# Optimization experiments

Hardware: AMD Instinct MI355X
Metric: run time of the kernel (lower is better)

Reference implementation:

```python
import jax, jax.numpy as jnp
import numpy as np

B, IN_DIM, HID = 32768, 512, 1024
# fixed triangle graph buffer from the module
SRC = jnp.array([0, 1, 2, 1, 2, 0], dtype=jnp.int32)
TGT = jnp.array([1, 2, 0, 0, 1, 2], dtype=jnp.int32)


def setup_inputs() -> dict:
    key = jax.random.key(0)
    ks = jax.random.split(key, 16)
    s_in = 1.0 / np.sqrt(IN_DIM)
    s_h = 1.0 / np.sqrt(HID)
    return {
        "x": jax.random.normal(ks[0], (B, IN_DIM), jnp.float32),
        # encoder: Linear(IN,HID) -> ReLU -> Linear(HID,HID) -> ReLU
        "enc_w1": jax.random.uniform(ks[1], (IN_DIM, HID), jnp.float32, -s_in, s_in),
        "enc_b1": jax.random.uniform(ks[2], (HID,), jnp.float32, -s_in, s_in),
        "enc_w2": jax.random.uniform(ks[3], (HID, HID), jnp.float32, -s_h, s_h),
        "enc_b2": jax.random.uniform(ks[4], (HID,), jnp.float32, -s_h, s_h),
        "init_nodes": jax.random.normal(ks[5], (3, HID), jnp.float32),
        # GIN layer 1 MLP: Linear -> ReLU -> Linear
        "gin1_w1": jax.random.uniform(ks[6], (HID, HID), jnp.float32, -s_h, s_h),
        "gin1_b1": jax.random.uniform(ks[7], (HID,), jnp.float32, -s_h, s_h),
        "gin1_w2": jax.random.uniform(ks[8], (HID, HID), jnp.float32, -s_h, s_h),
        "gin1_b2": jax.random.uniform(ks[9], (HID,), jnp.float32, -s_h, s_h),
        # GIN layer 2 MLP
        "gin2_w1": jax.random.uniform(ks[10], (HID, HID), jnp.float32, -s_h, s_h),
        "gin2_b1": jax.random.uniform(ks[11], (HID,), jnp.float32, -s_h, s_h),
        "gin2_w2": jax.random.uniform(ks[12], (HID, HID), jnp.float32, -s_h, s_h),
        "gin2_b2": jax.random.uniform(ks[13], (HID,), jnp.float32, -s_h, s_h),
        # decoder: Linear(HID, 1)
        "dec_w": jax.random.uniform(ks[14], (HID, 1), jnp.float32, -s_h, s_h),
        "dec_b": jax.random.uniform(ks[15], (1,), jnp.float32, -s_h, s_h),
    }


def _gin_conv(h, w1, b1, w2, b2):
    # h: [B, 3, H]; sum-aggregate neighbor features along fixed edge list, eps=0
    agg = jnp.zeros_like(h).at[:, TGT, :].add(h[:, SRC, :])
    m = h + agg  # (1+eps)*x + aggregate, eps=0
    m = jax.nn.relu(jnp.einsum('bnh,hk->bnk', m, w1) + b1)
    return jnp.einsum('bnh,hk->bnk', m, w2) + b2


def reference(x, enc_w1, enc_b1, enc_w2, enc_b2, init_nodes,
              gin1_w1, gin1_b1, gin1_w2, gin1_b2,
              gin2_w1, gin2_b1, gin2_w2, gin2_b2,
              dec_w, dec_b):
    # encoder (vectorized over batch)
    e = jax.nn.relu(x @ enc_w1 + enc_b1)
    e = jax.nn.relu(e @ enc_w2 + enc_b2)  # [B, H]
    # per-sample node init, batched: [B, 3, H]
    h = init_nodes[None, :, :] + e[:, None, :]
    h = jax.nn.relu(_gin_conv(h, gin1_w1, gin1_b1, gin1_w2, gin1_b2))
    h = jax.nn.relu(_gin_conv(h, gin2_w1, gin2_b1, gin2_w2, gin2_b2))
    out = (jnp.einsum('bnh,ho->bno', h, dec_w) + dec_b)[..., 0]  # [B, 3]
    return out
```

## Files before the change

### kernel.cpp

```cpp
#include <hip/hip_runtime.h>
#include <stdint.h>

#define AS1 __attribute__((address_space(1)))
#define AS3 __attribute__((address_space(3)))

typedef unsigned short ushort_t;
typedef __attribute__((ext_vector_type(8))) short bf16x8;
typedef __attribute__((ext_vector_type(4))) float f32x4;

__device__ __forceinline__ ushort_t f2bf(float f) {
  union { float f; uint32_t u; } c; c.f = f;
  uint32_t u = c.u;
  return (ushort_t)((u + 0x7fffu + ((u >> 16) & 1u)) >> 16);
}


__global__ __launch_bounds__(256) void k_cvt4(const float* __restrict__ in,
                                              ushort_t* __restrict__ out, int n4) {
  int i = blockIdx.x * blockDim.x + threadIdx.x;
  int stride = gridDim.x * blockDim.x;
  for (; i < n4; i += stride) {
    float4 v = ((const float4*)in)[i];
    ushort4 o;
    o.x = f2bf(v.x); o.y = f2bf(v.y); o.z = f2bf(v.z); o.w = f2bf(v.w);
    ((ushort4*)out)[i] = o;
  }
}

__global__ __launch_bounds__(256) void k_suminit(const float* __restrict__ init,
                                                 float* __restrict__ s) {
  int i = blockIdx.x * 256 + threadIdx.x;
  if (i < 1024) s[i] = init[i] + init[i + 1024] + init[i + 2048];
}

__global__ __launch_bounds__(256) void k_transpose(const float* __restrict__ W,
                                                   ushort_t* __restrict__ Wt,
                                                   int K, int N) {
  __shared__ float tile[32][33];
  int tx = threadIdx.x & 31, ty = threadIdx.x >> 5;
  int n0 = blockIdx.x * 32, k0 = blockIdx.y * 32;
  #pragma unroll
  for (int i = ty; i < 32; i += 8)
    tile[i][tx] = W[(size_t)(k0 + i) * N + (n0 + tx)];
  __syncthreads();
  #pragma unroll
  for (int i = ty; i < 32; i += 8)
    Wt[(size_t)(n0 + i) * K + (k0 + tx)] = f2bf(tile[tx][i]);
}


template <int KT, int EPI>
__global__ __launch_bounds__(256, 2)
void gemm_bt(const ushort_t* __restrict__ A, const ushort_t* __restrict__ Bt,
             const float* __restrict__ bias, const float* __restrict__ extra,
             ushort_t* __restrict__ C, float* __restrict__ part) {
  __shared__ char smem[32768];
  char* smA = smem;
  char* smB = smem + 16384;

  const int nwg = gridDim.x;
  const int cpx = nwg >> 3;
  int bid = blockIdx.x;
  int wg = (bid & 7) * cpx + (bid >> 3);
  const int mt = wg >> 3;
  const int nt = wg & 7;

  const int t = threadIdx.x;
  const int wave = t >> 6;
  const int lane = t & 63;
  const int wr = wave >> 1, wc = wave & 1;
  const int lrow = lane & 15;
  const int kq = lane >> 4;

  const char* Abase = (const char*)A + (size_t)mt * 128 * (KT * 2);
  const char* Bbase = (const char*)Bt + (size_t)nt * 128 * (KT * 2);

  const int rbase = wave * 8 + (lane >> 3);
  const int colOff = ((lane & 7) ^ (rbase & 7)) << 4;

  f32x4 acc[4][4];
  #pragma unroll
  for (int m = 0; m < 4; ++m)
    #pragma unroll
    for (int n = 0; n < 4; ++n)
      acc[m][n] = (f32x4){0.f, 0.f, 0.f, 0.f};

  constexpr int NKT = KT / 64;
  for (int kt = 0; kt < NKT; ++kt) {
    const size_t kb = (size_t)kt * 128;
    #pragma unroll
    for (int i = 0; i < 4; ++i) {
      int r = i * 32 + rbase;
      __builtin_amdgcn_global_load_lds(
          (const AS1 void*)(Abase + (size_t)r * (KT * 2) + kb + colOff),
          (AS3 void*)(smA + i * 4096 + wave * 1024), 16, 0, 0);
      __builtin_amdgcn_global_load_lds(
          (const AS1 void*)(Bbase + (size_t)r * (KT * 2) + kb + colOff),
          (AS3 void*)(smB + i * 4096 + wave * 1024), 16, 0, 0);
    }
    __syncthreads();
    #pragma unroll
    for (int ks = 0; ks < 2; ++ks) {
      bf16x8 af[4], bfv[4];
      #pragma unroll
      for (int m = 0; m < 4; ++m) {
        int r = wr * 64 + m * 16 + lrow;
        af[m] = *(const bf16x8*)(smA + r * 128 +
                                 ((ks * 64 + kq * 16) ^ ((r & 7) << 4)));
      }
      #pragma unroll
      for (int n = 0; n < 4; ++n) {
        int r = wc * 64 + n * 16 + lrow;
        bfv[n] = *(const bf16x8*)(smB + r * 128 +
                                  ((ks * 64 + kq * 16) ^ ((r & 7) << 4)));
      }
      #pragma unroll
      for (int m = 0; m < 4; ++m)
        #pragma unroll
        for (int n = 0; n < 4; ++n)
          acc[m][n] = __builtin_amdgcn_mfma_f32_16x16x32_bf16(af[m], bfv[n],
                                                              acc[m][n], 0, 0, 0);
    }
    __syncthreads();
  }

  const int row0 = mt * 128 + wr * 64;
  const int col0 = nt * 128 + wc * 64;
  if (EPI == 3) {
    float s[4][4];
    #pragma unroll
    for (int m = 0; m < 4; ++m)
      #pragma unroll
      for (int j = 0; j < 4; ++j) s[m][j] = 0.f;
    #pragma unroll
    for (int n = 0; n < 4; ++n) {
      int col = col0 + n * 16 + lrow;
      float bn = bias[col];
      float wn = extra[col];
      #pragma unroll
      for (int m = 0; m < 4; ++m)
        #pragma unroll
        for (int j = 0; j < 4; ++j) {
          float v = fmaxf(acc[m][n][j] + bn, 0.f);
          s[m][j] += v * wn;
        }
    }
    const int slot = nt * 2 + wc;
    #pragma unroll
    for (int m = 0; m < 4; ++m)
      #pragma unroll
      for (int j = 0; j < 4; ++j) {
        float v = s[m][j];
        v += __shfl_xor(v, 1);
        v += __shfl_xor(v, 2);
        v += __shfl_xor(v, 4);
        v += __shfl_xor(v, 8);
        if (lrow == 0)
          part[(size_t)slot * 32768 + (row0 + m * 16 + kq * 4 + j)] = v;
      }
  } else {
    float bn[4], en[4];
    #pragma unroll
    for (int n = 0; n < 4; ++n) {
      int col = col0 + n * 16 + lrow;
      bn[n] = bias[col];
      en[n] = (EPI == 1) ? extra[col] : 0.f;
    }
    #pragma unroll
    for (int m = 0; m < 4; ++m) {
      #pragma unroll
      for (int j = 0; j < 4; ++j) {
        int rb = row0 + m * 16 + kq * 4 + j;
        ushort_t* Crow = C + (size_t)rb * 1024 + col0 + lrow;
        #pragma unroll
        for (int n = 0; n < 4; ++n) {
          float v = acc[m][n][j] + bn[n];
          v = fmaxf(v, 0.f);
          if (EPI == 1) v = 3.f * v + en[n];
          else if (EPI == 2) v = 3.f * v;
          Crow[n * 16] = f2bf(v);
        }
      }
    }
  }
}


__global__ __launch_bounds__(256) void k_decfinal(const float* __restrict__ part,
                                                  const float* __restrict__ db,
                                                  float* __restrict__ out) {
  int r = blockIdx.x * 256 + threadIdx.x;
  float s = 0.f;
  #pragma unroll
  for (int i = 0; i < 16; ++i) s += part[(size_t)i * 32768 + r];
  float v = s + db[0];
  out[r * 3 + 0] = v;
  out[r * 3 + 1] = v;
  out[r * 3 + 2] = v;
}


extern "C" void kernel_launch(void* const* d_in, const int* in_sizes, int n_in,
                              void* d_out, int out_size, void* d_ws, size_t ws_size,
                              hipStream_t stream) {
  const float* x      = (const float*)d_in[0];
  const float* enc_w1 = (const float*)d_in[1];
  const float* enc_b1 = (const float*)d_in[2];
  const float* enc_w2 = (const float*)d_in[3];
  const float* enc_b2 = (const float*)d_in[4];
  const float* initn  = (const float*)d_in[5];
  const float* g1w1   = (const float*)d_in[6];
  const float* g1b1   = (const float*)d_in[7];
  const float* g1w2   = (const float*)d_in[8];
  const float* g1b2   = (const float*)d_in[9];
  const float* g2w1   = (const float*)d_in[10];
  const float* g2b1   = (const float*)d_in[11];
  const float* g2w2   = (const float*)d_in[12];
  const float* g2b2   = (const float*)d_in[13];
  const float* dec_w  = (const float*)d_in[14];
  const float* dec_b  = (const float*)d_in[15];
  float* out = (float*)d_out;

  char* ws = (char*)d_ws;
  ushort_t* xb    = (ushort_t*)(ws + 0);
  ushort_t* wtE1  = (ushort_t*)(ws + 33554432);
  ushort_t* wtE2  = (ushort_t*)(ws + 34603008);
  ushort_t* wtG11 = (ushort_t*)(ws + 36700160);
  ushort_t* wtG12 = (ushort_t*)(ws + 38797312);
  ushort_t* wtG21 = (ushort_t*)(ws + 40894464);
  ushort_t* wtG22 = (ushort_t*)(ws + 42991616);
  float*    sInit = (float*)   (ws + 45088768);
  ushort_t* bufA  = (ushort_t*)(ws + 45092864);
  ushort_t* bufB  = (ushort_t*)(ws + 112201728);
  float*    part  = (float*)   (ws + 112201728);

  k_cvt4<<<2048, 256, 0, stream>>>(x, xb, 32768 * 512 / 4);
  k_suminit<<<4, 256, 0, stream>>>(initn, sInit);
  {
    dim3 g512(32, 16), g1024(32, 32);
    k_transpose<<<g512, 256, 0, stream>>>(enc_w1, wtE1, 512, 1024);
    k_transpose<<<g1024, 256, 0, stream>>>(enc_w2, wtE2, 1024, 1024);
    k_transpose<<<g1024, 256, 0, stream>>>(g1w1, wtG11, 1024, 1024);
    k_transpose<<<g1024, 256, 0, stream>>>(g1w2, wtG12, 1024, 1024);
    k_transpose<<<g1024, 256, 0, stream>>>(g2w1, wtG21, 1024, 1024);
    k_transpose<<<g1024, 256, 0, stream>>>(g2w2, wtG22, 1024, 1024);
  }

  gemm_bt<512, 0><<<2048, 256, 0, stream>>>(xb, wtE1, enc_b1, nullptr, bufA, nullptr);
  gemm_bt<1024, 1><<<2048, 256, 0, stream>>>(bufA, wtE2, enc_b2, sInit, bufB, nullptr);
  gemm_bt<1024, 0><<<2048, 256, 0, stream>>>(bufB, wtG11, g1b1, nullptr, bufA, nullptr);
  gemm_bt<1024, 2><<<2048, 256, 0, stream>>>(bufA, wtG12, g1b2, nullptr, bufB, nullptr);
  gemm_bt<1024, 0><<<2048, 256, 0, stream>>>(bufB, wtG21, g2b1, nullptr, bufA, nullptr);
  gemm_bt<1024, 3><<<2048, 256, 0, stream>>>(bufA, wtG22, g2b2, dec_w, nullptr, part);
  k_decfinal<<<128, 256, 0, stream>>>(part, dec_b, out);
}
```

Before: 379.4 us.

## Fuse fp32-to-bf16 input conversion into first GEMM and batch weight transposes

The separate kernel that converted x to bf16 is removed; the first encoder GEMM now reads fp32 rows directly, converts them in registers and writes the swizzled tile into LDS. The six weight-transpose launches are merged into one 3D-grid launch that picks source and destination by blockIdx.z. Launch bounds move from 2 to 4 waves per SIMD. This removes a full write and re-read of the bf16 copy of x and several launch gaps, at the cost of synchronous fp32 loads in the first GEMM instead of async direct-to-LDS loads, and tighter register limits.

```diff
diff --git a/kernel.cpp b/kernel.cpp
--- a/kernel.cpp
+++ b/kernel.cpp
@@ -15,43 +15,44 @@
 }
 
 
-__global__ __launch_bounds__(256) void k_cvt4(const float* __restrict__ in,
-                                              ushort_t* __restrict__ out, int n4) {
-  int i = blockIdx.x * blockDim.x + threadIdx.x;
-  int stride = gridDim.x * blockDim.x;
-  for (; i < n4; i += stride) {
-    float4 v = ((const float4*)in)[i];
-    ushort4 o;
-    o.x = f2bf(v.x); o.y = f2bf(v.y); o.z = f2bf(v.z); o.w = f2bf(v.w);
-    ((ushort4*)out)[i] = o;
-  }
-}
-
 __global__ __launch_bounds__(256) void k_suminit(const float* __restrict__ init,
                                                  float* __restrict__ s) {
   int i = blockIdx.x * 256 + threadIdx.x;
   if (i < 1024) s[i] = init[i] + init[i + 1024] + init[i + 2048];
 }
 
-__global__ __launch_bounds__(256) void k_transpose(const float* __restrict__ W,
-                                                   ushort_t* __restrict__ Wt,
-                                                   int K, int N) {
+__global__ __launch_bounds__(256) void k_prep_w(
+    const float* s0, const float* s1, const float* s2, const float* s3,
+    const float* s4, const float* s5,
+    ushort_t* d0, ushort_t* d1, ushort_t* d2, ushort_t* d3,
+    ushort_t* d4, ushort_t* d5) {
+  const float* S; ushort_t* D; int K = 1024;
+  switch (blockIdx.z) {
+    case 0: S = s0; D = d0; K = 512; break;
+    case 1: S = s1; D = d1; break;
+    case 2: S = s2; D = d2; break;
+    case 3: S = s3; D = d3; break;
+    case 4: S = s4; D = d4; break;
+    default: S = s5; D = d5; break;
+  }
+  int k0 = blockIdx.y * 32;
+  if (k0 >= K) return;
   __shared__ float tile[32][33];
   int tx = threadIdx.x & 31, ty = threadIdx.x >> 5;
-  int n0 = blockIdx.x * 32, k0 = blockIdx.y * 32;
+  int n0 = blockIdx.x * 32;
   #pragma unroll
   for (int i = ty; i < 32; i += 8)
-    tile[i][tx] = W[(size_t)(k0 + i) * N + (n0 + tx)];
+    tile[i][tx] = S[(size_t)(k0 + i) * 1024 + (n0 + tx)];
   __syncthreads();
   #pragma unroll
   for (int i = ty; i < 32; i += 8)
-    Wt[(size_t)(n0 + i) * K + (k0 + tx)] = f2bf(tile[tx][i]);
-}
-
-
-template <int KT, int EPI>
-__global__ __launch_bounds__(256, 2)
-void gemm_bt(const ushort_t* __restrict__ A, const ushort_t* __restrict__ Bt,
+    D[(size_t)(n0 + i) * K + (k0 + tx)] = f2bf(tile[tx][i]);
+}
+
+
+template <int KT, int EPI, bool AF32>
+__global__ __launch_bounds__(256, 4)
+void gemm_bt(const void* __restrict__ Av, const ushort_t* __restrict__ Bt,
              const float* __restrict__ bias, const float* __restrict__ extra,
              ushort_t* __restrict__ C, float* __restrict__ part) {
   __shared__ char smem[32768];
@@ -72,11 +73,13 @@
   const int lrow = lane & 15;
   const int kq = lane >> 4;
 
-  const char* Abase = (const char*)A + (size_t)mt * 128 * (KT * 2);
+  const char* Abase = (const char*)Av +
+      (size_t)mt * 128 * (AF32 ? KT * 4 : KT * 2);
   const char* Bbase = (const char*)Bt + (size_t)nt * 128 * (KT * 2);
 
   const int rbase = wave * 8 + (lane >> 3);
-  const int colOff = ((lane & 7) ^ (rbase & 7)) << 4;
+  const int c16 = (lane & 7) ^ (rbase & 7);
+  const int colOff = c16 << 4;
 
   f32x4 acc[4][4];
   #pragma unroll
@@ -87,15 +90,27 @@
 
   constexpr int NKT = KT / 64;
   for (int kt = 0; kt < NKT; ++kt) {
-    const size_t kb = (size_t)kt * 128;
     #pragma unroll
     for (int i = 0; i < 4; ++i) {
       int r = i * 32 + rbase;
+      if constexpr (AF32) {
+        const char* src = Abase + (size_t)r * (KT * 4) + (size_t)kt * 256 +
+                          (c16 << 5);
+        float4 f0 = *(const float4*)(src);
+        float4 f1 = *(const float4*)(src + 16);
+        union { ushort_t us[8]; bf16x8 v; } pk;
+        pk.us[0] = f2bf(f0.x); pk.us[1] = f2bf(f0.y);
+        pk.us[2] = f2bf(f0.z); pk.us[3] = f2bf(f0.w);
+        pk.us[4] = f2bf(f1.x); pk.us[5] = f2bf(f1.y);
+        pk.us[6] = f2bf(f1.z); pk.us[7] = f2bf(f1.w);
+        *(bf16x8*)(smA + i * 4096 + wave * 1024 + lane * 16) = pk.v;
+      } else {
+        __builtin_amdgcn_global_load_lds(
+            (const AS1 void*)(Abase + (size_t)r * (KT * 2) + (size_t)kt * 128 + colOff),
+            (AS3 void*)(smA + i * 4096 + wave * 1024), 16, 0, 0);
+      }
       __builtin_amdgcn_global_load_lds(
-          (const AS1 void*)(Abase + (size_t)r * (KT * 2) + kb + colOff),
-          (AS3 void*)(smA + i * 4096 + wave * 1024), 16, 0, 0);
-      __builtin_amdgcn_global_load_lds(
-          (const AS1 void*)(Bbase + (size_t)r * (KT * 2) + kb + colOff),
+          (const AS1 void*)(Bbase + (size_t)r * (KT * 2) + (size_t)kt * 128 + colOff),
           (AS3 void*)(smB + i * 4096 + wave * 1024), 16, 0, 0);
     }
     __syncthreads();
@@ -222,7 +237,6 @@
   float* out = (float*)d_out;
 
   char* ws = (char*)d_ws;
-  ushort_t* xb    = (ushort_t*)(ws + 0);
   ushort_t* wtE1  = (ushort_t*)(ws + 33554432);
   ushort_t* wtE2  = (ushort_t*)(ws + 34603008);
   ushort_t* wtG11 = (ushort_t*)(ws + 36700160);
@@ -234,23 +248,18 @@
   ushort_t* bufB  = (ushort_t*)(ws + 112201728);
   float*    part  = (float*)   (ws + 112201728);
 
-  k_cvt4<<<2048, 256, 0, stream>>>(x, xb, 32768 * 512 / 4);
   k_suminit<<<4, 256, 0, stream>>>(initn, sInit);
   {
-    dim3 g512(32, 16), g1024(32, 32);
-    k_transpose<<<g512, 256, 0, stream>>>(enc_w1, wtE1, 512, 1024);
-    k_transpose<<<g1024, 256, 0, stream>>>(enc_w2, wtE2, 1024, 1024);
-    k_transpose<<<g1024, 256, 0, stream>>>(g1w1, wtG11, 1024, 1024);
-    k_transpose<<<g1024, 256, 0, stream>>>(g1w2, wtG12, 1024, 1024);
-    k_transpose<<<g1024, 256, 0, stream>>>(g2w1, wtG21, 1024, 1024);
-    k_transpose<<<g1024, 256, 0, stream>>>(g2w2, wtG22, 1024, 1024);
-  }
-
-  gemm_bt<512, 0><<<2048, 256, 0, stream>>>(xb, wtE1, enc_b1, nullptr, bufA, nullptr);
-  gemm_bt<1024, 1><<<2048, 256, 0, stream>>>(bufA, wtE2, enc_b2, sInit, bufB, nullptr);
-  gemm_bt<1024, 0><<<2048, 256, 0, stream>>>(bufB, wtG11, g1b1, nullptr, bufA, nullptr);
-  gemm_bt<1024, 2><<<2048, 256, 0, stream>>>(bufA, wtG12, g1b2, nullptr, bufB, nullptr);
-  gemm_bt<1024, 0><<<2048, 256, 0, stream>>>(bufB, wtG21, g2b1, nullptr, bufA, nullptr);
-  gemm_bt<1024, 3><<<2048, 256, 0, stream>>>(bufA, wtG22, g2b2, dec_w, nullptr, part);
+    dim3 g(32, 32, 6);
+    k_prep_w<<<g, 256, 0, stream>>>(enc_w1, enc_w2, g1w1, g1w2, g2w1, g2w2,
+                                    wtE1, wtE2, wtG11, wtG12, wtG21, wtG22);
+  }
+
+  gemm_bt<512, 0, true><<<2048, 256, 0, stream>>>(x, wtE1, enc_b1, nullptr, bufA, nullptr);
+  gemm_bt<1024, 1, false><<<2048, 256, 0, stream>>>(bufA, wtE2, enc_b2, sInit, bufB, nullptr);
+  gemm_bt<1024, 0, false><<<2048, 256, 0, stream>>>(bufB, wtG11, g1b1, nullptr, bufA, nullptr);
+  gemm_bt<1024, 2, false><<<2048, 256, 0, stream>>>(bufA, wtG12, g1b2, nullptr, bufB, nullptr);
+  gemm_bt<1024, 0, false><<<2048, 256, 0, stream>>>(bufB, wtG21, g2b1, nullptr, bufA, nullptr);
+  gemm_bt<1024, 3, false><<<2048, 256, 0, stream>>>(bufA, wtG22, g2b2, dec_w, nullptr, part);
   k_decfinal<<<128, 256, 0, stream>>>(part, dec_b, out);
 }
```

Measured after the change: 378.3 us. No clear change (-0.3%).
